# Performance work log

Hardware: AMD Instinct MI355X
Metric: run time of the kernel (lower is better)

## Reference

```python
import jax, jax.numpy as jnp
import numpy as np

S_LEN, BATCH, D, HK, M, L, VOCAB = 1024, 4, 1024, 1024, 4096, 6, 32000
EPS = 1e-5


def layernorm(x, g, b):
    mu = x.mean(-1, keepdims=True)
    xc = x - mu
    var = (xc * xc).mean(-1, keepdims=True)
    return xc * jax.lax.rsqrt(var + EPS) * g + b


def block(z, wq, wk, wv, wc, g1, bb1, w1, b1, w2, b2, g2, bb2):
    # Faithful to the torch block: permute (1,0,2) at entry, never permute back.
    x = jnp.swapaxes(z, 0, 1)  # [B', S', d]
    d = x.shape[-1]
    Q = jnp.einsum('bsd,ed->bse', x, wq)
    K = jnp.einsum('bsd,ed->bse', x, wk)
    V = jnp.einsum('bsd,ed->bse', x, wv)
    # NOTE: scale is sqrt(embed_dim)=sqrt(d), not sqrt(k); no causal mask (faithful).
    scores = jnp.einsum('bse,bte->bst', Q, K) / jnp.sqrt(jnp.asarray(d, x.dtype))
    A = jax.nn.softmax(scores, axis=-1)
    ctx = jnp.einsum('bst,bte->bse', A, V)
    att = jnp.einsum('bse,de->bsd', ctx, wc) + x
    h = layernorm(att, g1, bb1)
    # NOTE: no nonlinearity in the FFN (faithful to the source).
    f = jnp.einsum('bsd,md->bsm', h, w1) + b1
    f = jnp.einsum('bsm,dm->bsd', f, w2) + b2
    return layernorm(f + h, g2, bb2)


def forward(x, word_emb, pos_emb, wq, wk, wv, wc, ln1_g, ln1_b, w1, b1, w2, b2,
            ln2_g, ln2_b, dec_w, dec_b, out_bias):
    S = x.shape[0]
    z = word_emb[x] * jnp.sqrt(jnp.asarray(D, word_emb.dtype))  # [S,B,d]
    z = jax.nn.relu(z + pos_emb[jnp.arange(S)][:, None, :])
    for i in range(L):  # small fixed layer count; shapes alternate layout so no scan
        z = block(z, wq[i], wk[i], wv[i], wc[i], ln1_g[i], ln1_b[i],
                  w1[i], b1[i], w2[i], b2[i], ln2_g[i], ln2_b[i])
    logits = jnp.einsum('sbd,vd->sbv', z, dec_w) + dec_b + out_bias
    return jax.nn.log_softmax(logits, axis=-1)


def setup_inputs() -> dict:
    key = jax.random.key(0)
    ks = jax.random.split(key, 16)
    std = jnp.float32(0.02)
    return {
        'x': jax.random.randint(ks[0], (S_LEN, BATCH), 0, VOCAB),
        'word_emb': jax.random.normal(ks[1], (VOCAB, D), jnp.float32) * std,
        'pos_emb': jax.random.normal(ks[2], (S_LEN, D), jnp.float32) * std,
        'wq': jax.random.normal(ks[3], (L, HK, D), jnp.float32) * std,
        'wk': jax.random.normal(ks[4], (L, HK, D), jnp.float32) * std,
        'wv': jax.random.normal(ks[5], (L, HK, D), jnp.float32) * std,
        'wc': jax.random.normal(ks[6], (L, D, HK), jnp.float32) * std,
        'ln1_g': jnp.ones((L, D), jnp.float32),
        'ln1_b': jnp.zeros((L, D), jnp.float32),
        'w1': jax.random.normal(ks[7], (L, M, D), jnp.float32) * std,
        'b1': jnp.zeros((L, M), jnp.float32),
        'w2': jax.random.normal(ks[8], (L, D, M), jnp.float32) * std,
        'b2': jnp.zeros((L, D), jnp.float32),
        'ln2_g': jnp.ones((L, D), jnp.float32),
        'ln2_b': jnp.zeros((L, D), jnp.float32),
        'dec_w': jax.random.normal(ks[9], (VOCAB, D), jnp.float32) * std,
        'dec_b': jnp.zeros((VOCAB,), jnp.float32),
        'out_bias': jnp.zeros((VOCAB,), jnp.float32),
    }


def reference(x, word_emb, pos_emb, wq, wk, wv, wc, ln1_g, ln1_b, w1, b1, w2, b2,
              ln2_g, ln2_b, dec_w, dec_b, out_bias):
    return forward(x, word_emb, pos_emb, wq, wk, wv, wc, ln1_g, ln1_b, w1, b1,
                   w2, b2, ln2_g, ln2_b, dec_w, dec_b, out_bias)
```

## Files before the change

### kernel.cpp

```cpp
#include <hip/hip_runtime.h>

typedef short short8 __attribute__((ext_vector_type(8)));
typedef float f32x4 __attribute__((ext_vector_type(4)));

#define DMODEL 1024
#define HKDIM 1024
#define MDIM 4096
#define NROW 4096
#define VOCAB 32000
#define NLAYER 6

#define GLOAD_LDS16(g, l)                                                      \
  __builtin_amdgcn_global_load_lds(                                            \
      (const __attribute__((address_space(1))) void*)(g),                      \
      (__attribute__((address_space(3))) void*)(l), 16, 0, 0)

#define BARRIER_RAW()                      \
  do {                                     \
    __builtin_amdgcn_s_barrier();          \
    __builtin_amdgcn_sched_barrier(0);     \
  } while (0)
#define LGKM0()                                         \
  do {                                                  \
    asm volatile("s_waitcnt lgkmcnt(0)" ::: "memory");  \
    __builtin_amdgcn_sched_barrier(0);                  \
  } while (0)

__device__ __forceinline__ unsigned short f2bf(float f) {
  unsigned u = __float_as_uint(f);
  u += 0x7fffu + ((u >> 16) & 1u);
  return (unsigned short)(u >> 16);
}
__device__ __forceinline__ float bf2f(unsigned short h) {
  return __uint_as_float(((unsigned)h) << 16);
}
__device__ __forceinline__ float wave_sum(float v) {
  for (int o = 32; o; o >>= 1) v += __shfl_xor(v, o);
  return v;
}
__device__ __forceinline__ float wave_max(float v) {
  for (int o = 32; o; o >>= 1) v = fmaxf(v, __shfl_xor(v, o));
  return v;
}

__global__ __launch_bounds__(256) void k_embed(const int* __restrict__ x,
    const float* __restrict__ wemb, const float* __restrict__ pemb,
    float* __restrict__ z) {
  int r = blockIdx.x;
  int s = r >> 2;
  int tok = x[r];
  float4 a = ((const float4*)(wemb + (long)tok * DMODEL))[threadIdx.x];
  float4 p = ((const float4*)(pemb + (long)s * DMODEL))[threadIdx.x];
  float4 o;
  o.x = fmaxf(a.x * 32.0f + p.x, 0.0f);
  o.y = fmaxf(a.y * 32.0f + p.y, 0.0f);
  o.z = fmaxf(a.z * 32.0f + p.z, 0.0f);
  o.w = fmaxf(a.w * 32.0f + p.w, 0.0f);
  ((float4*)(z + (long)r * DMODEL))[threadIdx.x] = o;
}

__global__ __launch_bounds__(256) void k_permute(const float* __restrict__ zin,
    float* __restrict__ xf, unsigned short* __restrict__ xb, int A0, int A1) {
  int r = blockIdx.x;
  int a1 = r / A0, a0 = r - a1 * A0;
  float4 v = ((const float4*)(zin + (long)(a0 * A1 + a1) * DMODEL))[threadIdx.x];
  ((float4*)(xf + (long)r * DMODEL))[threadIdx.x] = v;
  ushort4 o = make_ushort4(f2bf(v.x), f2bf(v.y), f2bf(v.z), f2bf(v.w));
  ((ushort4*)(xb + (long)r * DMODEL))[threadIdx.x] = o;
}

__global__ __launch_bounds__(256) void k_cvt(const float* __restrict__ in,
    unsigned short* __restrict__ out, int n4) {
  int i = blockIdx.x * 256 + threadIdx.x;
  int stride = gridDim.x * 256;
  for (; i < n4; i += stride) {
    float4 v = ((const float4*)in)[i];
    ((ushort4*)out)[i] = make_ushort4(f2bf(v.x), f2bf(v.y), f2bf(v.z), f2bf(v.w));
  }
}

__global__ __launch_bounds__(256) void k_gemm_bt(
    const unsigned short* __restrict__ A, const unsigned short* __restrict__ B,
    float* __restrict__ Cf, unsigned short* __restrict__ Cb,
    const float* __restrict__ bias, const float* __restrict__ res,
    int M, int N, int K, int lda, int ldb, int ldc,
    long aB, long bB, long cB, float scale) {
  __shared__ unsigned short As[128 * 64];
  __shared__ unsigned short Bs[128 * 64];
  const int tid = threadIdx.x;
  const int gx = gridDim.x, gy = gridDim.y;

  int nwg = gx * gy * gridDim.z;
  int flat = blockIdx.x + gx * (blockIdx.y + gy * blockIdx.z);
  int q8 = nwg >> 3, r8 = nwg & 7;
  int xcd = flat & 7, inner = flat >> 3;
  int wg = (xcd < r8 ? xcd * (q8 + 1) : r8 * (q8 + 1) + (xcd - r8) * q8) + inner;
  int ty = wg % gy;
  int rest = wg / gy;
  int tx = rest % gx;
  int tz = rest / gx;

  const unsigned short* Ab = A + (long)tz * aB;
  const unsigned short* Bb = B + (long)tz * bB;
  const int row0 = ty * 128, col0 = tx * 128;
  const int lane = tid & 63, w = tid >> 6;
  const int wm = w >> 1, wn = w & 1;
  const int fr = lane & 15, fg = lane >> 4, fr7 = fr & 7;
  const int lrow = lane >> 3;
  const int lcol = ((lane & 7) ^ lrow) * 8;

  const unsigned short* aSrc = Ab + (long)(row0 + w * 32 + lrow) * lda + lcol;
  const unsigned short* bSrc = Bb + (long)(col0 + w * 32 + lrow) * ldb + lcol;
  unsigned short* aDst = As + w * 32 * 64;
  unsigned short* bDst = Bs + w * 32 * 64;

  f32x4 acc[4][4];
#pragma unroll
  for (int i = 0; i < 4; ++i)
#pragma unroll
    for (int j = 0; j < 4; ++j)
#pragma unroll
      for (int qq = 0; qq < 4; ++qq) acc[i][j][qq] = 0.0f;

  for (int k0 = 0; k0 < K; k0 += 64) {
#pragma unroll
    for (int i = 0; i < 4; ++i) {
      GLOAD_LDS16(aSrc + (long)i * 8 * lda + k0, aDst + i * 512);
      GLOAD_LDS16(bSrc + (long)i * 8 * ldb + k0, bDst + i * 512);
    }
    __syncthreads();
#pragma unroll
    for (int kk = 0; kk < 64; kk += 32) {
      short8 af[4], bfr[4];
#pragma unroll
      for (int i = 0; i < 4; ++i) {
        af[i] = *(const short8*)(As + (wm * 64 + i * 16 + fr) * 64 +
                                 (((kk >> 3) + fg) ^ fr7) * 8);
        bfr[i] = *(const short8*)(Bs + (wn * 64 + i * 16 + fr) * 64 +
                                  (((kk >> 3) + fg) ^ fr7) * 8);
      }
#pragma unroll
      for (int i = 0; i < 4; ++i)
#pragma unroll
        for (int j = 0; j < 4; ++j)
          acc[i][j] = __builtin_amdgcn_mfma_f32_16x16x32_bf16(af[i], bfr[j], acc[i][j], 0, 0, 0);
    }
    __syncthreads();
  }

#pragma unroll
  for (int j = 0; j < 4; ++j) {
    int col = col0 + wn * 64 + j * 16 + fr;
    float bv = bias ? bias[col] : 0.0f;
#pragma unroll
    for (int i = 0; i < 4; ++i) {
#pragma unroll
      for (int qq = 0; qq < 4; ++qq) {
        int row = row0 + wm * 64 + i * 16 + fg * 4 + qq;
        long off = cB * tz + (long)row * ldc + col;
        float v = acc[i][j][qq] * scale + bv;
        if (res) v += res[off];
        if (Cf) Cf[off] = v;
        if (Cb) Cb[off] = f2bf(v);
      }
    }
  }
}

__global__ __launch_bounds__(512, 2) void k_gemm8(
    const unsigned short* __restrict__ A, const unsigned short* __restrict__ B,
    float* __restrict__ Cf, unsigned short* __restrict__ Cb,
    const float* __restrict__ bias, int M, int N, int K,
    int lda, int ldb, int ldc) {
  __shared__ unsigned short As[2][256 * 64];
  __shared__ unsigned short Bs[2][256 * 64];
  const int tid = threadIdx.x;
  const int gx = gridDim.x, gy = gridDim.y;
  int nwg = gx * gy;
  int flat = blockIdx.x + gx * blockIdx.y;
  int q8 = nwg >> 3, r8 = nwg & 7;
  int xcd = flat & 7, inner = flat >> 3;
  int wg = (xcd < r8 ? xcd * (q8 + 1) : r8 * (q8 + 1) + (xcd - r8) * q8) + inner;
  int ty = wg % gy, tx = wg / gy;

  const int row0 = ty * 256, col0 = tx * 256;
  const int lane = tid & 63, w = tid >> 6;
  const int wm = w >> 2, wn = w & 3;
  const int fr = lane & 15, fg = lane >> 4, fr7 = fr & 7;
  const int srow = lane >> 3;
  const int scol = ((lane & 7) ^ srow) * 8;

  auto stage = [&](const unsigned short* __restrict__ mat, int ld, int rbase,
                   int tk, unsigned short* lds, int half) {
    const unsigned short* s =
        mat + (size_t)(rbase + half * 128 + w * 8 + srow) * ld + tk * 64 + scol;
    GLOAD_LDS16(s, lds + (half * 128 + w * 8) * 64);
    GLOAD_LDS16(s + (size_t)64 * ld, lds + (half * 128 + 64 + w * 8) * 64);
  };
  auto rdA = [&](const unsigned short* lds, int i, int kq) -> short8 {
    return *(const short8*)(lds + (wm * 128 + i * 16 + fr) * 64 +
                            (((kq << 2) + fg) ^ fr7) * 8);
  };
  auto rdB = [&](const unsigned short* lds, int j, int kq) -> short8 {
    return *(const short8*)(lds + (wn * 64 + j * 16 + fr) * 64 +
                            (((kq << 2) + fg) ^ fr7) * 8);
  };

  f32x4 acc[8][4];
#pragma unroll
  for (int i = 0; i < 8; ++i)
#pragma unroll
    for (int j = 0; j < 4; ++j)
#pragma unroll
      for (int qq = 0; qq < 4; ++qq) acc[i][j][qq] = 0.0f;

  short8 a8[8], b8[8];

#define RDA4(LDS, I0)                           \
  _Pragma("unroll") for (int i = 0; i < 4; ++i) { \
    a8[i * 2] = rdA(LDS, (I0) + i, 0);          \
    a8[i * 2 + 1] = rdA(LDS, (I0) + i, 1);      \
  }
#define RDB2(LDS, J0)                           \
  _Pragma("unroll") for (int j = 0; j < 2; ++j) { \
    b8[((J0) + j) * 2] = rdB(LDS, (J0) + j, 0); \
    b8[((J0) + j) * 2 + 1] = rdB(LDS, (J0) + j, 1); \
  }
#define MM8(I0, J0)                                                          \
  {                                                                          \
    __builtin_amdgcn_s_setprio(1);                                           \
    _Pragma("unroll") for (int i = 0; i < 4; ++i)                            \
      _Pragma("unroll") for (int j = 0; j < 2; ++j)                          \
        _Pragma("unroll") for (int kq = 0; kq < 2; ++kq)                     \
          acc[(I0) + i][(J0) + j] = __builtin_amdgcn_mfma_f32_16x16x32_bf16( \
              a8[i * 2 + kq], b8[((J0) + j) * 2 + kq],                       \
              acc[(I0) + i][(J0) + j], 0, 0, 0);                             \
    __builtin_amdgcn_s_setprio(0);                                           \
  }

  const int NT = K >> 6;

  stage(B, ldb, col0, 0, Bs[0], 0);
  stage(A, lda, row0, 0, As[0], 0);
  stage(A, lda, row0, 0, As[0], 1);
  stage(B, ldb, col0, 0, Bs[0], 1);
  stage(B, ldb, col0, 1, Bs[1], 0);
  stage(A, lda, row0, 1, As[1], 0);
  asm volatile("s_waitcnt vmcnt(4)" ::: "memory");
  BARRIER_RAW();

  for (int t = 0; t < NT; t += 2) {
    const bool more = (t + 2 < NT);
    RDA4(As[0], 0)
    RDB2(Bs[0], 0)
    stage(A, lda, row0, t + 1, As[1], 1);
    BARRIER_RAW(); LGKM0();
    MM8(0, 0)
    BARRIER_RAW();
    RDB2(Bs[0], 2)
    stage(B, ldb, col0, t + 1, Bs[1], 1);
    BARRIER_RAW(); LGKM0();
    MM8(0, 2)
    BARRIER_RAW();
    RDA4(As[0], 4)
    if (more) stage(B, ldb, col0, t + 2, Bs[0], 0);
    BARRIER_RAW(); LGKM0();
    MM8(4, 0)
    BARRIER_RAW();
    if (more) {
      stage(A, lda, row0, t + 2, As[0], 0);
      asm volatile("s_waitcnt vmcnt(4)" ::: "memory");
    } else {
      asm volatile("s_waitcnt vmcnt(0)" ::: "memory");
    }
    BARRIER_RAW(); LGKM0();
    MM8(4, 2)
    BARRIER_RAW();
    RDA4(As[1], 0)
    RDB2(Bs[1], 0)
    if (more) stage(A, lda, row0, t + 2, As[0], 1);
    BARRIER_RAW(); LGKM0();
    MM8(0, 0)
    BARRIER_RAW();
    RDB2(Bs[1], 2)
    if (more) stage(B, ldb, col0, t + 2, Bs[0], 1);
    BARRIER_RAW(); LGKM0();
    MM8(0, 2)
    BARRIER_RAW();
    RDA4(As[1], 4)
    if (more) stage(B, ldb, col0, t + 3, Bs[1], 0);
    BARRIER_RAW(); LGKM0();
    MM8(4, 0)
    BARRIER_RAW();
    if (more) {
      stage(A, lda, row0, t + 3, As[1], 0);
      asm volatile("s_waitcnt vmcnt(4)" ::: "memory");
    } else {
      asm volatile("s_waitcnt vmcnt(0)" ::: "memory");
    }
    BARRIER_RAW(); LGKM0();
    MM8(4, 2)
    BARRIER_RAW();
  }

#pragma unroll
  for (int j = 0; j < 4; ++j) {
    int col = col0 + wn * 64 + j * 16 + fr;
    float bv = bias ? bias[col] : 0.0f;
#pragma unroll
    for (int i = 0; i < 8; ++i) {
#pragma unroll
      for (int qq = 0; qq < 4; ++qq) {
        int row = row0 + wm * 128 + i * 16 + fg * 4 + qq;
        size_t off = (size_t)row * ldc + col;
        float v = acc[i][j][qq] + bv;
        if (Cf) Cf[off] = v;
        if (Cb) Cb[off] = f2bf(v);
      }
    }
  }
#undef RDA4
#undef RDB2
#undef MM8
}

__global__ __launch_bounds__(256) void k_ln(const float* __restrict__ X,
    const float* __restrict__ X2, const float* __restrict__ g,
    const float* __restrict__ b, float* __restrict__ outF,
    unsigned short* __restrict__ outB) {
  __shared__ float sm[4];
  int row = blockIdx.x, t = threadIdx.x;
  float4 v = ((const float4*)(X + (long)row * DMODEL))[t];
  if (X2) {
    float4 u = ((const float4*)(X2 + (long)row * DMODEL))[t];
    v.x += u.x; v.y += u.y; v.z += u.z; v.w += u.w;
  }
  float s = wave_sum(v.x + v.y + v.z + v.w);
  if ((t & 63) == 0) sm[t >> 6] = s;
  __syncthreads();
  float mean = (sm[0] + sm[1] + sm[2] + sm[3]) * (1.0f / DMODEL);
  __syncthreads();
  float4 c;
  c.x = v.x - mean; c.y = v.y - mean; c.z = v.z - mean; c.w = v.w - mean;
  float ss = wave_sum(c.x * c.x + c.y * c.y + c.z * c.z + c.w * c.w);
  if ((t & 63) == 0) sm[t >> 6] = ss;
  __syncthreads();
  float var = (sm[0] + sm[1] + sm[2] + sm[3]) * (1.0f / DMODEL);
  float rs = rsqrtf(var + 1e-5f);
  float4 gv = ((const float4*)g)[t], bv = ((const float4*)b)[t];
  float4 o;
  o.x = c.x * rs * gv.x + bv.x;
  o.y = c.y * rs * gv.y + bv.y;
  o.z = c.z * rs * gv.z + bv.z;
  o.w = c.w * rs * gv.w + bv.w;
  if (outF) ((float4*)(outF + (long)row * DMODEL))[t] = o;
  if (outB)
    ((ushort4*)(outB + (long)row * DMODEL))[t] =
        make_ushort4(f2bf(o.x), f2bf(o.y), f2bf(o.z), f2bf(o.w));
}

__global__ __launch_bounds__(256) void k_softmax(const float* __restrict__ S,
    unsigned short* __restrict__ A) {
  __shared__ float sm[4];
  int row = blockIdx.x, t = threadIdx.x;
  float4 v = ((const float4*)(S + (long)row * 1024))[t];
  float m = wave_max(fmaxf(fmaxf(v.x, v.y), fmaxf(v.z, v.w)));
  if ((t & 63) == 0) sm[t >> 6] = m;
  __syncthreads();
  m = fmaxf(fmaxf(sm[0], sm[1]), fmaxf(sm[2], sm[3]));
  __syncthreads();
  float4 e;
  e.x = __expf(v.x - m); e.y = __expf(v.y - m);
  e.z = __expf(v.z - m); e.w = __expf(v.w - m);
  float s = wave_sum(e.x + e.y + e.z + e.w);
  if ((t & 63) == 0) sm[t >> 6] = s;
  __syncthreads();
  float inv = 1.0f / (sm[0] + sm[1] + sm[2] + sm[3]);
  ((ushort4*)(A + (long)row * 1024))[t] =
      make_ushort4(f2bf(e.x * inv), f2bf(e.y * inv), f2bf(e.z * inv), f2bf(e.w * inv));
}

__global__ __launch_bounds__(256) void k_attn4(const unsigned short* __restrict__ QKV,
    unsigned short* __restrict__ C) {
  int bp = blockIdx.x;
  int w = threadIdx.x >> 6, lane = threadIdx.x & 63;
  const unsigned short* q = QKV + (long)(bp * 4 + w) * 3072;
  float s[4];
  for (int j = 0; j < 4; ++j) {
    const unsigned short* kj = QKV + (long)(bp * 4 + j) * 3072 + 1024;
    float a = 0.0f;
    for (int e = lane; e < 1024; e += 64) a += bf2f(q[e]) * bf2f(kj[e]);
    s[j] = wave_sum(a) * (1.0f / 32.0f);
  }
  float m = fmaxf(fmaxf(s[0], s[1]), fmaxf(s[2], s[3]));
  float e0 = __expf(s[0] - m), e1 = __expf(s[1] - m);
  float e2 = __expf(s[2] - m), e3 = __expf(s[3] - m);
  float inv = 1.0f / (e0 + e1 + e2 + e3);
  float a0 = e0 * inv, a1 = e1 * inv, a2 = e2 * inv, a3 = e3 * inv;
  unsigned short* c = C + (long)(bp * 4 + w) * 1024;
  const unsigned short* v0 = QKV + (long)(bp * 4 + 0) * 3072 + 2048;
  const unsigned short* v1 = QKV + (long)(bp * 4 + 1) * 3072 + 2048;
  const unsigned short* v2 = QKV + (long)(bp * 4 + 2) * 3072 + 2048;
  const unsigned short* v3 = QKV + (long)(bp * 4 + 3) * 3072 + 2048;
  for (int e = lane; e < 1024; e += 64) {
    float v = a0 * bf2f(v0[e]) + a1 * bf2f(v1[e]) + a2 * bf2f(v2[e]) + a3 * bf2f(v3[e]);
    c[e] = f2bf(v);
  }
}

__global__ __launch_bounds__(256) void k_transpose(const unsigned short* __restrict__ in,
    unsigned short* __restrict__ out, int rows, int cols, int ld_in, int ld_out,
    long inB, long outB) {
  __shared__ unsigned short tile[32][33];
  long ibase = (long)blockIdx.z * inB;
  long obase = (long)blockIdx.z * outB;
  int r0 = blockIdx.y * 32, c0 = blockIdx.x * 32;
  int tx = threadIdx.x, ty = threadIdx.y;
  for (int i = ty; i < 32; i += 8)
    tile[i][tx] = in[ibase + (long)(r0 + i) * ld_in + c0 + tx];
  __syncthreads();
  for (int i = ty; i < 32; i += 8)
    out[obase + (long)(c0 + i) * ld_out + r0 + tx] = tile[tx][i];
}

__global__ __launch_bounds__(320) void k_logsoftmax(float* __restrict__ L) {
  __shared__ float sm[5];
  int row = blockIdx.x, t = threadIdx.x;
  float* x = L + (long)row * VOCAB;
  float4 v[25];
  float m = -1e30f;
#pragma unroll
  for (int i = 0; i < 25; ++i) {
    v[i] = ((const float4*)x)[t + i * 320];
    m = fmaxf(m, fmaxf(fmaxf(v[i].x, v[i].y), fmaxf(v[i].z, v[i].w)));
  }
  m = wave_max(m);
  if ((t & 63) == 0) sm[t >> 6] = m;
  __syncthreads();
  m = fmaxf(fmaxf(fmaxf(sm[0], sm[1]), fmaxf(sm[2], sm[3])), sm[4]);
  __syncthreads();
  float s = 0.0f;
#pragma unroll
  for (int i = 0; i < 25; ++i)
    s += __expf(v[i].x - m) + __expf(v[i].y - m) + __expf(v[i].z - m) + __expf(v[i].w - m);
  s = wave_sum(s);
  if ((t & 63) == 0) sm[t >> 6] = s;
  __syncthreads();
  float l = m + __logf(sm[0] + sm[1] + sm[2] + sm[3] + sm[4]);
#pragma unroll
  for (int i = 0; i < 25; ++i) {
    float4 o = v[i];
    o.x -= l; o.y -= l; o.z -= l; o.w -= l;
    ((float4*)x)[t + i * 320] = o;
  }
}

__global__ __launch_bounds__(256) void k_addbias(const float* __restrict__ a,
    const float* __restrict__ b, float* __restrict__ o, int n) {
  int i = blockIdx.x * 256 + threadIdx.x;
  if (i < n) o[i] = a[i] + b[i];
}

extern "C" void kernel_launch(void* const* d_in, const int* in_sizes, int n_in,
                              void* d_out, int out_size, void* d_ws, size_t ws_size,
                              hipStream_t stream) {
  const int* x = (const int*)d_in[0];
  const float* wemb = (const float*)d_in[1];
  const float* pemb = (const float*)d_in[2];
  const float* wq = (const float*)d_in[3];
  const float* wk = (const float*)d_in[4];
  const float* wv = (const float*)d_in[5];
  const float* wc = (const float*)d_in[6];
  const float* ln1g = (const float*)d_in[7];
  const float* ln1b = (const float*)d_in[8];
  const float* w1 = (const float*)d_in[9];
  const float* b1 = (const float*)d_in[10];
  const float* w2 = (const float*)d_in[11];
  const float* b2 = (const float*)d_in[12];
  const float* ln2g = (const float*)d_in[13];
  const float* ln2b = (const float*)d_in[14];
  const float* decw = (const float*)d_in[15];
  const float* decb = (const float*)d_in[16];
  const float* obias = (const float*)d_in[17];
  float* out = (float*)d_out;

  char* ws = (char*)d_ws;
  size_t off = 0;
  auto alloc = [&](size_t bytes) -> char* {
    char* p = ws + off;
    off += (bytes + 255) & ~(size_t)255;
    return p;
  };
  float* z = (float*)alloc((size_t)NROW * DMODEL * 4);
  float* xf = (float*)alloc((size_t)NROW * DMODEL * 4);
  unsigned short* xb = (unsigned short*)alloc((size_t)NROW * DMODEL * 2);
  unsigned short* qkv = (unsigned short*)alloc((size_t)NROW * 3072 * 2);
  unsigned short* vt = (unsigned short*)alloc((size_t)NROW * HKDIM * 2);
  unsigned short* wbuf = (unsigned short*)alloc((size_t)MDIM * DMODEL * 2);
  float* tmp16 = (float*)alloc((size_t)NROW * 1024 * 4);
  unsigned short* am = (unsigned short*)alloc((size_t)NROW * 1024 * 2);
  unsigned short* ctx = (unsigned short*)alloc((size_t)NROW * HKDIM * 2);
  float* h = (float*)alloc((size_t)NROW * DMODEL * 4);
  unsigned short* hb = (unsigned short*)alloc((size_t)NROW * DMODEL * 2);
  unsigned short* f = (unsigned short*)alloc((size_t)NROW * MDIM * 2);
  unsigned short* dwb = (unsigned short*)alloc((size_t)VOCAB * DMODEL * 2);
  unsigned short* zb = (unsigned short*)alloc((size_t)NROW * DMODEL * 2);
  float* biasD = (float*)alloc((size_t)VOCAB * 4);
  (void)ws_size; (void)in_sizes; (void)n_in; (void)out_size;

  auto gemm = [&](const unsigned short* A, const unsigned short* B, float* Cf,
                  unsigned short* Cb, const float* bias, const float* res, int M,
                  int N, int K, int lda, int ldb, int ldc, int batch, long aB,
                  long bB, long cB, float scale) {
    dim3 g(N / 128, M / 128, batch);
    k_gemm_bt<<<g, dim3(256), 0, stream>>>(A, B, Cf, Cb, bias, res, M, N, K,
                                           lda, ldb, ldc, aB, bB, cB, scale);
  };
  auto gemm8 = [&](const unsigned short* A, const unsigned short* B, float* Cf,
                   unsigned short* Cb, const float* bias, int M, int N, int K,
                   int lda, int ldb, int ldc) {
    k_gemm8<<<dim3(N / 256, M / 256, 1), dim3(512), 0, stream>>>(
        A, B, Cf, Cb, bias, M, N, K, lda, ldb, ldc);
  };
  auto cvt = [&](const float* in, unsigned short* o, long n) {
    int n4 = (int)(n / 4);
    int grid = (n4 + 255) / 256;
    if (grid > 2048) grid = 2048;
    k_cvt<<<dim3(grid), dim3(256), 0, stream>>>(in, o, n4);
  };

  k_embed<<<NROW, 256, 0, stream>>>(x, wemb, pemb, z);

  for (int i = 0; i < NLAYER; ++i) {
    int A0 = (i % 2 == 0) ? 1024 : 4;
    int A1 = 4096 / A0;
    k_permute<<<NROW, 256, 0, stream>>>(z, xf, xb, A0, A1);

    cvt(wq + (long)i * HKDIM * DMODEL, wbuf, (long)HKDIM * DMODEL);
    cvt(wk + (long)i * HKDIM * DMODEL, wbuf + (size_t)1024 * DMODEL, (long)HKDIM * DMODEL);
    cvt(wv + (long)i * HKDIM * DMODEL, wbuf + (size_t)2048 * DMODEL, (long)HKDIM * DMODEL);
    gemm8(xb, wbuf, nullptr, qkv, nullptr, NROW, 3072, DMODEL, DMODEL, DMODEL, 3072);

    if (A0 == 1024) {
      gemm(qkv, qkv + 1024, tmp16, nullptr, nullptr, nullptr, 1024, 1024, 1024,
           3072, 3072, 1024, 4, (long)1024 * 3072, (long)1024 * 3072, 1 << 20,
           1.0f / 32.0f);
      k_softmax<<<NROW, 256, 0, stream>>>(tmp16, am);
      k_transpose<<<dim3(32, 32, 4), dim3(32, 8), 0, stream>>>(
          qkv + 2048, vt, 1024, 1024, 3072, 1024, (long)1024 * 3072, 1 << 20);
      gemm(am, vt, nullptr, ctx, nullptr, nullptr, 1024, 1024, 1024,
           1024, 1024, 1024, 4, 1 << 20, 1 << 20, 1 << 20, 1.0f);
    } else {
      k_attn4<<<1024, 256, 0, stream>>>(qkv, ctx);
    }

    cvt(wc + (long)i * DMODEL * HKDIM, wbuf, (long)DMODEL * HKDIM);
    gemm(ctx, wbuf, tmp16, nullptr, nullptr, xf, NROW, DMODEL, HKDIM,
         HKDIM, HKDIM, DMODEL, 1, 0, 0, 0, 1.0f);
    k_ln<<<NROW, 256, 0, stream>>>(tmp16, nullptr, ln1g + (long)i * DMODEL,
                                   ln1b + (long)i * DMODEL, h, hb);
    cvt(w1 + (long)i * MDIM * DMODEL, wbuf, (long)MDIM * DMODEL);
    gemm8(hb, wbuf, nullptr, f, b1 + (long)i * MDIM, NROW, MDIM, DMODEL,
          DMODEL, DMODEL, MDIM);
    cvt(w2 + (long)i * DMODEL * MDIM, wbuf, (long)DMODEL * MDIM);
    gemm(f, wbuf, tmp16, nullptr, b2 + (long)i * DMODEL, nullptr, NROW, DMODEL, MDIM,
         MDIM, MDIM, DMODEL, 1, 0, 0, 0, 1.0f);
    k_ln<<<NROW, 256, 0, stream>>>(tmp16, h, ln2g + (long)i * DMODEL,
                                   ln2b + (long)i * DMODEL, z, nullptr);
  }

  cvt(z, zb, (long)NROW * DMODEL);
  cvt(decw, dwb, (long)VOCAB * DMODEL);
  k_addbias<<<(VOCAB + 255) / 256, 256, 0, stream>>>(decb, obias, biasD, VOCAB);
  gemm8(zb, dwb, out, nullptr, biasD, NROW, VOCAB, DMODEL, DMODEL, DMODEL, VOCAB);
  k_logsoftmax<<<NROW, 320, 0, stream>>>(out);
}
```

Baseline: 2.479 ms.

## Restructure GEMM mainloop into quadrant-ordered ping-pong with deeper prefetch

Reworks the 256x256 bf16 GEMM main loop so each K-tile is consumed in four quadrant phases (A-lo/B-lo, A-lo/B-hi, A-hi/B-hi, A-hi/B-lo), reusing B fragments across phases. Global-to-LDS staging for the tile two steps ahead is issued into the buffer as soon as each quadrant of it has been read, and B rows are partitioned differently across waves. Both buffers are prefetched upfront, and the final iterations reload a clamped tile instead of branching. The goal is to overlap global loads with MFMA work and cut LDS reads and branches. In exchange, the barrier and waitcnt ordering is more intricate, and the clamped tail does redundant loads.

```diff
diff --git a/kernel.cpp b/kernel.cpp
--- a/kernel.cpp
+++ b/kernel.cpp
@@ -189,13 +189,14 @@
   const int fr = lane & 15, fg = lane >> 4, fr7 = fr & 7;
   const int srow = lane >> 3;
   const int scol = ((lane & 7) ^ srow) * 8;
-
-  auto stage = [&](const unsigned short* __restrict__ mat, int ld, int rbase,
-                   int tk, unsigned short* lds, int half) {
-    const unsigned short* s =
-        mat + (size_t)(rbase + half * 128 + w * 8 + srow) * ld + tk * 64 + scol;
-    GLOAD_LDS16(s, lds + (half * 128 + w * 8) * 64);
-    GLOAD_LDS16(s + (size_t)64 * ld, lds + (half * 128 + 64 + w * 8) * 64);
+  const int bq = (w >> 1) * 64 + (w & 1) * 16;
+
+  const unsigned short* pA = A + (size_t)(row0 + srow) * lda + scol;
+  const unsigned short* pB = B + (size_t)(col0 + srow) * ldb + scol;
+
+  auto stg = [&](const unsigned short* base, int ld, int tk,
+                 unsigned short* lds, int r0) {
+    GLOAD_LDS16(base + (size_t)r0 * ld + (size_t)tk * 64, lds + r0 * 64);
   };
   auto rdA = [&](const unsigned short* lds, int i, int kq) -> short8 {
     return *(const short8*)(lds + (wm * 128 + i * 16 + fr) * 64 +
@@ -214,94 +215,84 @@
 #pragma unroll
       for (int qq = 0; qq < 4; ++qq) acc[i][j][qq] = 0.0f;
 
-  short8 a8[8], b8[8];
-
-#define RDA4(LDS, I0)                           \
-  _Pragma("unroll") for (int i = 0; i < 4; ++i) { \
-    a8[i * 2] = rdA(LDS, (I0) + i, 0);          \
-    a8[i * 2 + 1] = rdA(LDS, (I0) + i, 1);      \
-  }
-#define RDB2(LDS, J0)                           \
-  _Pragma("unroll") for (int j = 0; j < 2; ++j) { \
-    b8[((J0) + j) * 2] = rdB(LDS, (J0) + j, 0); \
-    b8[((J0) + j) * 2 + 1] = rdB(LDS, (J0) + j, 1); \
-  }
-#define MM8(I0, J0)                                                          \
+  short8 a8[8], bLo[4], bHi[4];
+
+#define ST_A_LO(bf, tk) { stg(pA, lda, tk, As[bf], w * 8); stg(pA, lda, tk, As[bf], 128 + w * 8); }
+#define ST_B_LO(bf, tk) { stg(pB, ldb, tk, Bs[bf], bq); stg(pB, ldb, tk, Bs[bf], bq + 8); }
+#define ST_B_HI(bf, tk) { stg(pB, ldb, tk, Bs[bf], bq + 32); stg(pB, ldb, tk, Bs[bf], bq + 40); }
+#define ST_A_HI(bf, tk) { stg(pA, lda, tk, As[bf], 64 + w * 8); stg(pA, lda, tk, As[bf], 192 + w * 8); }
+
+#define RD_ALO(bf)                                  \
+  _Pragma("unroll") for (int i = 0; i < 4; ++i) {   \
+    a8[i * 2] = rdA(As[bf], i, 0);                  \
+    a8[i * 2 + 1] = rdA(As[bf], i, 1);              \
+  }
+#define RD_AHI(bf)                                  \
+  _Pragma("unroll") for (int i = 0; i < 4; ++i) {   \
+    a8[i * 2] = rdA(As[bf], i + 4, 0);              \
+    a8[i * 2 + 1] = rdA(As[bf], i + 4, 1);          \
+  }
+#define RD_BLO(bf)                                  \
+  _Pragma("unroll") for (int j = 0; j < 2; ++j) {   \
+    bLo[j * 2] = rdB(Bs[bf], j, 0);                 \
+    bLo[j * 2 + 1] = rdB(Bs[bf], j, 1);             \
+  }
+#define RD_BHI(bf)                                  \
+  _Pragma("unroll") for (int j = 0; j < 2; ++j) {   \
+    bHi[j * 2] = rdB(Bs[bf], j + 2, 0);             \
+    bHi[j * 2 + 1] = rdB(Bs[bf], j + 2, 1);         \
+  }
+#define MFMA_Q(I0, BREG, J0)                                                 \
   {                                                                          \
     __builtin_amdgcn_s_setprio(1);                                           \
-    _Pragma("unroll") for (int i = 0; i < 4; ++i)                            \
-      _Pragma("unroll") for (int j = 0; j < 2; ++j)                          \
-        _Pragma("unroll") for (int kq = 0; kq < 2; ++kq)                     \
+    _Pragma("unroll") for (int kq = 0; kq < 2; ++kq)                         \
+      _Pragma("unroll") for (int i = 0; i < 4; ++i)                          \
+        _Pragma("unroll") for (int j = 0; j < 2; ++j)                        \
           acc[(I0) + i][(J0) + j] = __builtin_amdgcn_mfma_f32_16x16x32_bf16( \
-              a8[i * 2 + kq], b8[((J0) + j) * 2 + kq],                       \
+              a8[i * 2 + kq], BREG[j * 2 + kq],                              \
               acc[(I0) + i][(J0) + j], 0, 0, 0);                             \
     __builtin_amdgcn_s_setprio(0);                                           \
   }
 
+#define TILE8(BF, TP)                                        \
+                                                 \
+  RD_ALO(BF) RD_BLO(BF)                                      \
+  BARRIER_RAW(); LGKM0();                                    \
+  MFMA_Q(0, bLo, 0)                                          \
+  BARRIER_RAW();                                             \
+                                                 \
+  RD_BHI(BF)                                                 \
+  ST_A_LO(BF, TP) ST_B_LO(BF, TP)                            \
+  BARRIER_RAW(); LGKM0();                                    \
+  MFMA_Q(0, bHi, 2)                                          \
+  BARRIER_RAW();                                             \
+                                                 \
+  RD_AHI(BF)                                                 \
+  ST_B_HI(BF, TP)                                            \
+  BARRIER_RAW(); LGKM0();                                    \
+  MFMA_Q(4, bHi, 2)                                          \
+  BARRIER_RAW();                                             \
+   \
+  ST_A_HI(BF, TP)                                            \
+  BARRIER_RAW();                                             \
+  MFMA_Q(4, bLo, 0)                                          \
+  asm volatile("s_waitcnt vmcnt(8)" ::: "memory");           \
+  BARRIER_RAW();
+
   const int NT = K >> 6;
 
-  stage(B, ldb, col0, 0, Bs[0], 0);
-  stage(A, lda, row0, 0, As[0], 0);
-  stage(A, lda, row0, 0, As[0], 1);
-  stage(B, ldb, col0, 0, Bs[0], 1);
-  stage(B, ldb, col0, 1, Bs[1], 0);
-  stage(A, lda, row0, 1, As[1], 0);
-  asm volatile("s_waitcnt vmcnt(4)" ::: "memory");
+  ST_A_LO(0, 0) ST_B_LO(0, 0) ST_B_HI(0, 0) ST_A_HI(0, 0)
+  ST_A_LO(1, 1) ST_B_LO(1, 1) ST_B_HI(1, 1) ST_A_HI(1, 1)
+  asm volatile("s_waitcnt vmcnt(8)" ::: "memory");
   BARRIER_RAW();
 
   for (int t = 0; t < NT; t += 2) {
-    const bool more = (t + 2 < NT);
-    RDA4(As[0], 0)
-    RDB2(Bs[0], 0)
-    stage(A, lda, row0, t + 1, As[1], 1);
-    BARRIER_RAW(); LGKM0();
-    MM8(0, 0)
-    BARRIER_RAW();
-    RDB2(Bs[0], 2)
-    stage(B, ldb, col0, t + 1, Bs[1], 1);
-    BARRIER_RAW(); LGKM0();
-    MM8(0, 2)
-    BARRIER_RAW();
-    RDA4(As[0], 4)
-    if (more) stage(B, ldb, col0, t + 2, Bs[0], 0);
-    BARRIER_RAW(); LGKM0();
-    MM8(4, 0)
-    BARRIER_RAW();
-    if (more) {
-      stage(A, lda, row0, t + 2, As[0], 0);
-      asm volatile("s_waitcnt vmcnt(4)" ::: "memory");
-    } else {
-      asm volatile("s_waitcnt vmcnt(0)" ::: "memory");
-    }
-    BARRIER_RAW(); LGKM0();
-    MM8(4, 2)
-    BARRIER_RAW();
-    RDA4(As[1], 0)
-    RDB2(Bs[1], 0)
-    if (more) stage(A, lda, row0, t + 2, As[0], 1);
-    BARRIER_RAW(); LGKM0();
-    MM8(0, 0)
-    BARRIER_RAW();
-    RDB2(Bs[1], 2)
-    if (more) stage(B, ldb, col0, t + 2, Bs[0], 1);
-    BARRIER_RAW(); LGKM0();
-    MM8(0, 2)
-    BARRIER_RAW();
-    RDA4(As[1], 4)
-    if (more) stage(B, ldb, col0, t + 3, Bs[1], 0);
-    BARRIER_RAW(); LGKM0();
-    MM8(4, 0)
-    BARRIER_RAW();
-    if (more) {
-      stage(A, lda, row0, t + 3, As[1], 0);
-      asm volatile("s_waitcnt vmcnt(4)" ::: "memory");
-    } else {
-      asm volatile("s_waitcnt vmcnt(0)" ::: "memory");
-    }
-    BARRIER_RAW(); LGKM0();
-    MM8(4, 2)
-    BARRIER_RAW();
-  }
+    int tp0 = (t + 2 < NT) ? t + 2 : NT - 1;
+    int tp1 = (t + 3 < NT) ? t + 3 : NT - 1;
+    TILE8(0, tp0)
+    TILE8(1, tp1)
+  }
+  asm volatile("s_waitcnt vmcnt(0)" ::: "memory");
 
 #pragma unroll
   for (int j = 0; j < 4; ++j) {
@@ -319,9 +310,16 @@
       }
     }
   }
-#undef RDA4
-#undef RDB2
-#undef MM8
+#undef TILE8
+#undef MFMA_Q
+#undef RD_ALO
+#undef RD_AHI
+#undef RD_BLO
+#undef RD_BHI
+#undef ST_A_LO
+#undef ST_A_HI
+#undef ST_B_LO
+#undef ST_B_HI
 }
 
 __global__ __launch_bounds__(256) void k_ln(const float* __restrict__ X,
```

New measurement: 2.514 ms. No clear change (+1.4%).
